# Kernel optimization log

Measured on AMD Instinct MI355X. Metric: run time of the kernel, lower is better.

Reference implementation:

```python
import jax, jax.numpy as jnp
import numpy as np

THRESHOLD = 0.25
W_CD, W_FID, W_NC, W_SYM, W_DIFF = 1.0, 0.5, 0.1, 0.1, 1.0
KL_BETA = 0.0  # _step = 0 at init -> kl_beta = beta_max * min(1, 0/5000) = 0


def _cdist(p1, p2):
    # torch.cdist(p=2): [B,N,3] x [B,M,3] -> [B,N,M]
    sq1 = jnp.sum(p1 * p1, axis=-1)  # [B,N]
    sq2 = jnp.sum(p2 * p2, axis=-1)  # [B,M]
    d2 = sq1[:, :, None] + sq2[:, None, :] - 2.0 * jnp.einsum('bnd,bmd->bnm', p1, p2)
    return jnp.sqrt(jnp.maximum(d2, 0.0))


def _chamfer_l1(p1, p2):
    dist = _cdist(p1, p2)
    cd = dist.min(axis=2).mean(axis=1) + dist.min(axis=1).mean(axis=1)
    return cd.mean()


def setup_inputs() -> dict:
    key = jax.random.key(0)
    ks = jax.random.split(key, 11)
    B, N, M, P, D = 4, 4096, 4096, 2048, 512
    pn = jax.random.normal(ks[7], (B, 3), dtype=jnp.float32)
    pn = pn / jnp.linalg.norm(pn, axis=-1, keepdims=True)  # unit plane normals
    return {
        'pred': jax.random.normal(ks[0], (B, N, 3), dtype=jnp.float32),
        'full': jax.random.normal(ks[1], (B, M, 3), dtype=jnp.float32),
        'partial': jax.random.normal(ks[2], (B, P, 3), dtype=jnp.float32),
        'mu': jax.random.normal(ks[3], (B, D), dtype=jnp.float32),
        'logvar': jax.random.normal(ks[4], (B, D), dtype=jnp.float32),
        'pred_normals': jax.random.normal(ks[5], (B, N, 3), dtype=jnp.float32),
        'gt_normals': jax.random.normal(ks[6], (B, N, 3), dtype=jnp.float32),
        'plane_normals': pn,
        'plane_offsets': jax.random.normal(ks[8], (B,), dtype=jnp.float32) * 0.1,
        'sym_confidences': jax.random.uniform(ks[9], (B,), dtype=jnp.float32),
        'diffusion_loss': jax.random.uniform(ks[10], (), dtype=jnp.float32),
    }


def reference(pred, full, partial, mu, logvar, pred_normals, gt_normals,
              plane_normals, plane_offsets, sym_confidences, diffusion_loss):
    # chamfer L1
    cd = _chamfer_l1(pred, full)
    # KL divergence of diagonal Gaussian
    kl = (-0.5 * (1.0 + logvar - mu * mu - jnp.exp(logvar))).sum(axis=-1).mean()
    # fidelity: partial -> pred nearest-neighbor distance
    fid = _cdist(partial, pred).min(axis=2).mean()
    # normal consistency: 1 - |cos|
    num = jnp.sum(pred_normals * gt_normals, axis=-1)
    den = jnp.linalg.norm(pred_normals, axis=-1) * jnp.linalg.norm(gt_normals, axis=-1)
    cos = num / jnp.maximum(den, 1e-8)
    nc = (1.0 - jnp.abs(cos)).mean()
    # bilateral symmetry error (confidence-gated), vectorized over batch
    off = jax.lax.stop_gradient(plane_offsets)  # torch uses .item() -> constant
    s = jnp.einsum('bnd,bd->bn', pred, plane_normals) + off[:, None]  # signed dist
    reflected = pred - 2.0 * s[..., None] * plane_normals[:, None, :]
    dist = _cdist(pred, reflected)
    cd_l1_b = dist.min(axis=2).mean(axis=1) + dist.min(axis=1).mean(axis=1)  # [B]
    sym_b = jnp.where(sym_confidences >= THRESHOLD,
                      sym_confidences * cd_l1_b * 0.5, 0.0)
    sym = sym_b.mean()
    total = (W_CD * cd + KL_BETA * kl + W_FID * fid + W_NC * nc
             + W_SYM * sym + W_DIFF * diffusion_loss)
    return total
```

## Files before the change

kernel.cpp:

```cpp
#include <hip/hip_runtime.h>

#define BB 4
#define NN 4096
#define PP 2048

#define HCAND 2048
#define QPT 8
#define QPB 32

#define NCOFF 114688
#define P2OFF 114752


__global__ __launch_bounds__(256, 4) void nn_kernel(
    const float* __restrict__ pred, const float* __restrict__ full,
    const float* __restrict__ partial, const float* __restrict__ plane_n,
    const float* __restrict__ plane_off,
    const float* __restrict__ pn, const float* __restrict__ gn,
    float* __restrict__ ws)
{
    int blk = blockIdx.x;
    int tid = threadIdx.x;
    __shared__ float4 sc[HCAND];
    __shared__ float sred[4];

    if (blk >= 3584) {
        int i = (blk - 3584) * 256 + tid;
        const float* p = pn + (size_t)i * 3;
        const float* g = gn + (size_t)i * 3;
        float px = p[0], py = p[1], pz = p[2];
        float gx = g[0], gy = g[1], gz = g[2];
        float num = fmaf(px, gx, fmaf(py, gy, pz * gz));
        float den = sqrtf(fmaf(px, px, fmaf(py, py, pz * pz))) *
                    sqrtf(fmaf(gx, gx, fmaf(gy, gy, gz * gz)));
        float v = 1.f - fabsf(num / fmaxf(den, 1e-8f));
        for (int o = 1; o < 64; o <<= 1) v += __shfl_xor(v, o);
        if ((tid & 63) == 0) sred[tid >> 6] = v;
        __syncthreads();
        if (tid == 0) ws[NCOFF + (blk - 3584)] = sred[0] + sred[1] + sred[2] + sred[3];
        return;
    }

    int half = blk & 1, t = blk >> 1;
    const float* cand; const float* qptr; int qsl; bool reflect = false; int b;
    if (t < 512) {
        b = t >> 7; int ch = t & 127;
        cand = full + (size_t)b * NN * 3;
        qptr = pred + ((size_t)b * NN + ch * QPB) * 3;
        qsl = b * 4096 + ch * QPB;
    } else if (t < 1024) {
        int u = t - 512; b = u >> 7; int ch = u & 127;
        cand = pred + (size_t)b * NN * 3;
        qptr = full + ((size_t)b * NN + ch * QPB) * 3;
        qsl = 16384 + b * 4096 + ch * QPB;
    } else if (t < 1280) {
        int u = t - 1024; b = u >> 6; int ch = u & 63;
        cand = pred + (size_t)b * NN * 3;
        qptr = partial + ((size_t)b * PP + ch * QPB) * 3;
        qsl = 32768 + b * 2048 + ch * QPB;
    } else {
        int u = t - 1280; b = u >> 7; int ch = u & 127;
        cand = pred + (size_t)b * NN * 3;
        qptr = pred + ((size_t)b * NN + ch * QPB) * 3;
        qsl = 40960 + b * 4096 + ch * QPB;
        reflect = true;
    }

    float nx = 0.f, ny = 0.f, nz = 0.f, noff = 0.f;
    if (reflect) {
        nx = plane_n[b * 3]; ny = plane_n[b * 3 + 1]; nz = plane_n[b * 3 + 2];
        noff = plane_off[b];
    }

    int cbase = half * HCAND;
#pragma unroll
    for (int r = 0; r < HCAND / 256; ++r) {
        const float* cp = cand + (size_t)(cbase + r * 256 + tid) * 3;
        float x = cp[0], y = cp[1], z = cp[2];
        if (reflect) {
            float sd = fmaf(x, nx, fmaf(y, ny, fmaf(z, nz, noff)));
            float t2 = 2.0f * sd;
            x -= t2 * nx; y -= t2 * ny; z -= t2 * nz;
        }
        sc[r * 256 + tid] = make_float4(x, y, z, fmaf(x, x, fmaf(y, y, z * z)));
    }
    __syncthreads();

    int lane = tid & 63;
    int wv = tid >> 6;
    float ax[QPT], ay[QPT], az[QPT], md[QPT];
#pragma unroll
    for (int j = 0; j < QPT; ++j) {
        const float* qp = qptr + (size_t)(wv * QPT + j) * 3;
        ax[j] = -2.f * qp[0]; ay[j] = -2.f * qp[1]; az[j] = -2.f * qp[2];
        md[j] = 3.4e38f;
    }

#pragma unroll 4
    for (int k = 0; k < HCAND / 128; ++k) {
        float4 ca = sc[k * 128 + lane];
        float4 cb = sc[k * 128 + 64 + lane];
#pragma unroll
        for (int j = 0; j < QPT; ++j) {
            float ta = fmaf(ax[j], ca.x, fmaf(ay[j], ca.y, fmaf(az[j], ca.z, ca.w)));
            float tb = fmaf(ax[j], cb.x, fmaf(ay[j], cb.y, fmaf(az[j], cb.z, cb.w)));
            md[j] = fminf(md[j], fminf(ta, tb));
        }
    }

#pragma unroll
    for (int j = 0; j < QPT; ++j) {
        md[j] = fminf(md[j], __shfl_xor(md[j], 1));
        md[j] = fminf(md[j], __shfl_xor(md[j], 2));
        md[j] = fminf(md[j], __shfl_xor(md[j], 4));
        md[j] = fminf(md[j], __shfl_xor(md[j], 8));
        md[j] = fminf(md[j], __shfl_xor(md[j], 16));
        md[j] = fminf(md[j], __shfl_xor(md[j], 32));
    }
    if (lane == 0) {
#pragma unroll
        for (int j = 0; j < QPT; ++j)
            ws[(size_t)(qsl + wv * QPT + j) * 2 + half] = md[j];
    }
}

__global__ __launch_bounds__(256) void pass2_kernel(
    const float* __restrict__ pred, const float* __restrict__ full,
    const float* __restrict__ partial, float* __restrict__ ws)
{
    int i = blockIdx.x * 256 + threadIdx.x;
    const float* q;
    if (i < 16384)       q = pred + (size_t)i * 3;
    else if (i < 32768)  q = full + (size_t)(i - 16384) * 3;
    else if (i < 40960)  q = partial + (size_t)(i - 32768) * 3;
    else                 q = pred + (size_t)(i - 40960) * 3;
    float m = fminf(ws[(size_t)i * 2], ws[(size_t)i * 2 + 1]);
    float x = q[0], y = q[1], z = q[2];
    float q2 = fmaf(x, x, fmaf(y, y, z * z));
    float d = sqrtf(fmaxf(q2 + m, 0.f));
    for (int o = 1; o < 64; o <<= 1) d += __shfl_xor(d, o);
    __shared__ float sred[4];
    int tid = threadIdx.x;
    if ((tid & 63) == 0) sred[tid >> 6] = d;
    __syncthreads();
    if (tid == 0)
        ws[P2OFF + blockIdx.x] = sred[0] + sred[1] + sred[2] + sred[3];
}

__global__ __launch_bounds__(256) void final_kernel(
    const float* __restrict__ ws,
    const float* __restrict__ confs,
    const float* __restrict__ diff,
    float* __restrict__ out)
{
    __shared__ float vals[224 + 64];
    int tid = threadIdx.x;
    if (tid < 224) vals[tid] = ws[P2OFF + tid];
    if (tid < 64) vals[224 + tid] = ws[NCOFF + tid];
    __syncthreads();
    if (tid == 0) {
        float seg[8];
        for (int s = 0; s < 8; ++s) seg[s] = 0.f;
        for (int i = 0; i < 64; ++i)  seg[0] += vals[i];
        for (int i = 64; i < 128; ++i) seg[1] += vals[i];
        for (int i = 128; i < 160; ++i) seg[2] += vals[i];
        for (int i = 160; i < 224; ++i) seg[3 + ((i - 160) >> 4)] += vals[i];
        for (int i = 0; i < 64; ++i)  seg[7] += vals[224 + i];
        const float BN = (float)(BB * NN);
        const float BP = (float)(BB * PP);
        float cd  = seg[0] / BN + seg[1] / BN;
        float fid = seg[2] / BP;
        float nc  = seg[7] / BN;
        float sym = 0.f;
#pragma unroll
        for (int b = 0; b < BB; ++b) {
            float conf = confs[b];
            if (conf >= 0.25f) {
                float cdl1 = 2.0f * seg[3 + b] / (float)NN;
                sym += conf * cdl1 * 0.5f;
            }
        }
        sym *= (1.0f / BB);
        out[0] = 1.0f * cd + 0.5f * fid + 0.1f * nc + 0.1f * sym + diff[0];
    }
}

extern "C" void kernel_launch(void* const* d_in, const int* in_sizes, int n_in,
                              void* d_out, int out_size, void* d_ws, size_t ws_size,
                              hipStream_t stream) {
    const float* pred      = (const float*)d_in[0];
    const float* full      = (const float*)d_in[1];
    const float* partial   = (const float*)d_in[2];
    const float* pred_n    = (const float*)d_in[5];
    const float* gt_n      = (const float*)d_in[6];
    const float* plane_n   = (const float*)d_in[7];
    const float* plane_off = (const float*)d_in[8];
    const float* confs     = (const float*)d_in[9];
    const float* diff      = (const float*)d_in[10];
    float* ws = (float*)d_ws;

    nn_kernel<<<3648, 256, 0, stream>>>(pred, full, partial, plane_n,
                                        plane_off, pred_n, gt_n, ws);
    pass2_kernel<<<224, 256, 0, stream>>>(pred, full, partial, ws);
    final_kernel<<<1, 256, 0, stream>>>(ws, confs, diff, (float*)d_out);
}
```

Baseline: 35.23 us.

## Use packed FMA over candidate pairs, full candidate set per block, fuse sqrt pass

Each block now scans all 4096 candidates, stored as interleaved pairs in shared memory (x0,x1,y0,y1 / z0,z1), and evaluates two candidates per packed FMA. Each thread now handles 16 queries instead of 8. The second pass (combining the halves plus sqrt) is folded into the nn kernel's epilogue, and the final kernel reduces per-wave partial sums using shared atomics. This removes one kernel launch and the workspace round trip, and roughly halves the issued FMA instructions. In exchange it recomputes candidate norms inside the loop, raises register pressure (launch bounds drop to 3), and launches fewer blocks (960).

Result: slower. 42.79 us (+21.5%).

```diff
diff --git a/kernel.cpp b/kernel.cpp
--- a/kernel.cpp
+++ b/kernel.cpp
@@ -4,28 +4,34 @@
 #define NN 4096
 #define PP 2048
 
-#define HCAND 2048
-#define QPT 8
-#define QPB 32
-
-#define NCOFF 114688
-#define P2OFF 114752
-
-
-__global__ __launch_bounds__(256, 4) void nn_kernel(
+#define NPAIR 2048
+#define QPT 16
+#define QPB 64
+
+typedef float f2 __attribute__((ext_vector_type(2)));
+
+#if __has_builtin(__builtin_elementwise_fma)
+#define PKFMA(a, b, c) __builtin_elementwise_fma((a), (b), (c))
+#else
+#define PKFMA(a, b, c) ((a) * (b) + (c))
+#endif
+
+
+__global__ __launch_bounds__(256, 3) void nn_kernel(
     const float* __restrict__ pred, const float* __restrict__ full,
     const float* __restrict__ partial, const float* __restrict__ plane_n,
     const float* __restrict__ plane_off,
     const float* __restrict__ pn, const float* __restrict__ gn,
-    float* __restrict__ ws)
+    float* __restrict__ res)
 {
     int blk = blockIdx.x;
     int tid = threadIdx.x;
-    __shared__ float4 sc[HCAND];
-    __shared__ float sred[4];
-
-    if (blk >= 3584) {
-        int i = (blk - 3584) * 256 + tid;
+    __shared__ float4 scx[NPAIR];
+    __shared__ float2 scz[NPAIR];
+
+    if (blk >= 896) {
+        __shared__ float sred[4];
+        int i = (blk - 896) * 256 + tid;
         const float* p = pn + (size_t)i * 3;
         const float* g = gn + (size_t)i * 3;
         float px = p[0], py = p[1], pz = p[2];
@@ -37,32 +43,27 @@
         for (int o = 1; o < 64; o <<= 1) v += __shfl_xor(v, o);
         if ((tid & 63) == 0) sred[tid >> 6] = v;
         __syncthreads();
-        if (tid == 0) ws[NCOFF + (blk - 3584)] = sred[0] + sred[1] + sred[2] + sred[3];
+        if (tid == 0) res[3584 + (blk - 896)] = sred[0] + sred[1] + sred[2] + sred[3];
         return;
     }
 
-    int half = blk & 1, t = blk >> 1;
-    const float* cand; const float* qptr; int qsl; bool reflect = false; int b;
-    if (t < 512) {
-        b = t >> 7; int ch = t & 127;
+    const float* cand; const float* qptr; bool reflect = false; int b;
+    if (blk < 256) {
+        b = blk >> 6; int ch = blk & 63;
         cand = full + (size_t)b * NN * 3;
         qptr = pred + ((size_t)b * NN + ch * QPB) * 3;
-        qsl = b * 4096 + ch * QPB;
-    } else if (t < 1024) {
-        int u = t - 512; b = u >> 7; int ch = u & 127;
+    } else if (blk < 512) {
+        int u = blk - 256; b = u >> 6; int ch = u & 63;
         cand = pred + (size_t)b * NN * 3;
         qptr = full + ((size_t)b * NN + ch * QPB) * 3;
-        qsl = 16384 + b * 4096 + ch * QPB;
-    } else if (t < 1280) {
-        int u = t - 1024; b = u >> 6; int ch = u & 63;
+    } else if (blk < 640) {
+        int u = blk - 512; b = u >> 5; int ch = u & 31;
         cand = pred + (size_t)b * NN * 3;
         qptr = partial + ((size_t)b * PP + ch * QPB) * 3;
-        qsl = 32768 + b * 2048 + ch * QPB;
     } else {
-        int u = t - 1280; b = u >> 7; int ch = u & 127;
+        int u = blk - 640; b = u >> 6; int ch = u & 63;
         cand = pred + (size_t)b * NN * 3;
         qptr = pred + ((size_t)b * NN + ch * QPB) * 3;
-        qsl = 40960 + b * 4096 + ch * QPB;
         reflect = true;
     }
 
@@ -72,39 +73,54 @@
         noff = plane_off[b];
     }
 
-    int cbase = half * HCAND;
-#pragma unroll
-    for (int r = 0; r < HCAND / 256; ++r) {
-        const float* cp = cand + (size_t)(cbase + r * 256 + tid) * 3;
-        float x = cp[0], y = cp[1], z = cp[2];
+#pragma unroll
+    for (int r = 0; r < NPAIR / 256; ++r) {
+        int p = r * 256 + tid;
+        const float* cp = cand + (size_t)p * 6;
+        float2 v0 = *(const float2*)(cp);
+        float2 v1 = *(const float2*)(cp + 2);
+        float2 v2 = *(const float2*)(cp + 4);
+        float x0 = v0.x, y0 = v0.y, z0 = v1.x;
+        float x1 = v1.y, y1 = v2.x, z1 = v2.y;
         if (reflect) {
-            float sd = fmaf(x, nx, fmaf(y, ny, fmaf(z, nz, noff)));
-            float t2 = 2.0f * sd;
-            x -= t2 * nx; y -= t2 * ny; z -= t2 * nz;
-        }
-        sc[r * 256 + tid] = make_float4(x, y, z, fmaf(x, x, fmaf(y, y, z * z)));
+            float s0 = fmaf(x0, nx, fmaf(y0, ny, fmaf(z0, nz, noff)));
+            float t0 = 2.0f * s0;
+            x0 -= t0 * nx; y0 -= t0 * ny; z0 -= t0 * nz;
+            float s1 = fmaf(x1, nx, fmaf(y1, ny, fmaf(z1, nz, noff)));
+            float t1 = 2.0f * s1;
+            x1 -= t1 * nx; y1 -= t1 * ny; z1 -= t1 * nz;
+        }
+        scx[p] = make_float4(x0, x1, y0, y1);
+        scz[p] = make_float2(z0, z1);
     }
     __syncthreads();
 
     int lane = tid & 63;
-    int wv = tid >> 6;
-    float ax[QPT], ay[QPT], az[QPT], md[QPT];
+    int wv = __builtin_amdgcn_readfirstlane(tid >> 6);
+    const float* qp = qptr + (size_t)wv * QPT * 3;
+    f2 qx2[QPT], qy2[QPT], qz2[QPT];
+    float md[QPT];
 #pragma unroll
     for (int j = 0; j < QPT; ++j) {
-        const float* qp = qptr + (size_t)(wv * QPT + j) * 3;
-        ax[j] = -2.f * qp[0]; ay[j] = -2.f * qp[1]; az[j] = -2.f * qp[2];
+        float qx = qp[j * 3], qy = qp[j * 3 + 1], qz = qp[j * 3 + 2];
+        qx2[j] = (f2){-2.f * qx, -2.f * qx};
+        qy2[j] = (f2){-2.f * qy, -2.f * qy};
+        qz2[j] = (f2){-2.f * qz, -2.f * qz};
         md[j] = 3.4e38f;
     }
 
-#pragma unroll 4
-    for (int k = 0; k < HCAND / 128; ++k) {
-        float4 ca = sc[k * 128 + lane];
-        float4 cb = sc[k * 128 + 64 + lane];
+#pragma unroll 8
+    for (int k = 0; k < NPAIR / 64; ++k) {
+        float4 cxy = scx[k * 64 + lane];
+        float2 czz = scz[k * 64 + lane];
+        f2 cx2 = (f2){cxy.x, cxy.y};
+        f2 cy2 = (f2){cxy.z, cxy.w};
+        f2 cz2 = (f2){czz.x, czz.y};
+        f2 cw2 = PKFMA(cz2, cz2, PKFMA(cy2, cy2, cx2 * cx2));
 #pragma unroll
         for (int j = 0; j < QPT; ++j) {
-            float ta = fmaf(ax[j], ca.x, fmaf(ay[j], ca.y, fmaf(az[j], ca.z, ca.w)));
-            float tb = fmaf(ax[j], cb.x, fmaf(ay[j], cb.y, fmaf(az[j], cb.z, cb.w)));
-            md[j] = fminf(md[j], fminf(ta, tb));
+            f2 t = PKFMA(cx2, qx2[j], PKFMA(cy2, qy2[j], PKFMA(cz2, qz2[j], cw2)));
+            md[j] = fminf(md[j], fminf(t.x, t.y));
         }
     }
 
@@ -118,54 +134,39 @@
         md[j] = fminf(md[j], __shfl_xor(md[j], 32));
     }
     if (lane == 0) {
-#pragma unroll
-        for (int j = 0; j < QPT; ++j)
-            ws[(size_t)(qsl + wv * QPT + j) * 2 + half] = md[j];
+        float s = 0.f;
+#pragma unroll
+        for (int j = 0; j < QPT; ++j) {
+            float qx = qp[j * 3], qy = qp[j * 3 + 1], qz = qp[j * 3 + 2];
+            float q2 = fmaf(qx, qx, fmaf(qy, qy, qz * qz));
+            s += sqrtf(fmaxf(q2 + md[j], 0.f));
+        }
+        res[blk * 4 + wv] = s;
     }
 }
 
-__global__ __launch_bounds__(256) void pass2_kernel(
-    const float* __restrict__ pred, const float* __restrict__ full,
-    const float* __restrict__ partial, float* __restrict__ ws)
-{
-    int i = blockIdx.x * 256 + threadIdx.x;
-    const float* q;
-    if (i < 16384)       q = pred + (size_t)i * 3;
-    else if (i < 32768)  q = full + (size_t)(i - 16384) * 3;
-    else if (i < 40960)  q = partial + (size_t)(i - 32768) * 3;
-    else                 q = pred + (size_t)(i - 40960) * 3;
-    float m = fminf(ws[(size_t)i * 2], ws[(size_t)i * 2 + 1]);
-    float x = q[0], y = q[1], z = q[2];
-    float q2 = fmaf(x, x, fmaf(y, y, z * z));
-    float d = sqrtf(fmaxf(q2 + m, 0.f));
-    for (int o = 1; o < 64; o <<= 1) d += __shfl_xor(d, o);
-    __shared__ float sred[4];
-    int tid = threadIdx.x;
-    if ((tid & 63) == 0) sred[tid >> 6] = d;
-    __syncthreads();
-    if (tid == 0)
-        ws[P2OFF + blockIdx.x] = sred[0] + sred[1] + sred[2] + sred[3];
-}
-
 __global__ __launch_bounds__(256) void final_kernel(
-    const float* __restrict__ ws,
+    const float* __restrict__ res,
     const float* __restrict__ confs,
     const float* __restrict__ diff,
     float* __restrict__ out)
 {
-    __shared__ float vals[224 + 64];
+    __shared__ float seg[8];
     int tid = threadIdx.x;
-    if (tid < 224) vals[tid] = ws[P2OFF + tid];
-    if (tid < 64) vals[224 + tid] = ws[NCOFF + tid];
+    if (tid < 8) seg[tid] = 0.f;
+    __syncthreads();
+    for (int i = tid; i < 3648; i += 256) {
+        float v = res[i];
+        int sgi;
+        if (i < 1024) sgi = 0;
+        else if (i < 2048) sgi = 1;
+        else if (i < 2560) sgi = 2;
+        else if (i < 3584) sgi = 3 + ((i - 2560) >> 8);
+        else sgi = 7;
+        atomicAdd(&seg[sgi], v);
+    }
     __syncthreads();
     if (tid == 0) {
-        float seg[8];
-        for (int s = 0; s < 8; ++s) seg[s] = 0.f;
-        for (int i = 0; i < 64; ++i)  seg[0] += vals[i];
-        for (int i = 64; i < 128; ++i) seg[1] += vals[i];
-        for (int i = 128; i < 160; ++i) seg[2] += vals[i];
-        for (int i = 160; i < 224; ++i) seg[3 + ((i - 160) >> 4)] += vals[i];
-        for (int i = 0; i < 64; ++i)  seg[7] += vals[224 + i];
         const float BN = (float)(BB * NN);
         const float BP = (float)(BB * PP);
         float cd  = seg[0] / BN + seg[1] / BN;
@@ -197,10 +198,9 @@
     const float* plane_off = (const float*)d_in[8];
     const float* confs     = (const float*)d_in[9];
     const float* diff      = (const float*)d_in[10];
-    float* ws = (float*)d_ws;
-
-    nn_kernel<<<3648, 256, 0, stream>>>(pred, full, partial, plane_n,
-                                        plane_off, pred_n, gt_n, ws);
-    pass2_kernel<<<224, 256, 0, stream>>>(pred, full, partial, ws);
-    final_kernel<<<1, 256, 0, stream>>>(ws, confs, diff, (float*)d_out);
+    float* res = (float*)d_ws;
+
+    nn_kernel<<<960, 256, 0, stream>>>(pred, full, partial, plane_n,
+                                       plane_off, pred_n, gt_n, res);
+    final_kernel<<<1, 256, 0, stream>>>(res, confs, diff, (float*)d_out);
 }
```
